# Kernel tuning notes

Hardware: AMD Instinct MI355X
Metric: run time of the kernel (lower is better)

Reference implementation:

```python
import jax, jax.numpy as jnp
import numpy as np

NEG_BIG = -9e15
ALPHA = 0.2  # leakyrelu slope


def setup_inputs() -> dict:
    key = jax.random.key(0)
    k1, k2, k3, k4 = jax.random.split(key, 4)
    N, Fin, Fout = 8192, 256, 256
    input = jax.random.normal(k1, (N, Fin), dtype=jnp.float32)
    adj = jax.random.randint(k2, (N, N), 0, 2, dtype=jnp.int32)
    W = jax.random.normal(k3, (Fin, Fout), dtype=jnp.float32) * (1.0 / np.sqrt(Fin))
    a = jax.random.normal(k4, (2 * Fout, 1), dtype=jnp.float32) * (1.0 / np.sqrt(Fout))
    return {"input": input, "adj": adj, "W": W, "a": a}


def reference(input, adj, W, a):
    # h: [N, F]
    h = input @ W
    Fout = h.shape[1]
    # Fused score: e_ij = leakyrelu(h_i . a[:F] + h_j . a[F:])
    s1 = h @ a[:Fout, 0]   # [N]
    s2 = h @ a[Fout:, 0]   # [N]
    e = s1[:, None] + s2[None, :]            # [N, N]
    e = jnp.where(e >= 0, e, ALPHA * e)      # leaky relu
    e = jnp.where(adj > 0, e, NEG_BIG)       # mask
    attention = jax.nn.softmax(e, axis=1)    # row softmax
    h_prime = attention @ h                  # [N, F]
    return jax.nn.elu(h_prime)               # concat=True -> elu
```

## Files before the change

### kernel.cpp

```cpp
#include <hip/hip_runtime.h>
#include <hip/hip_bf16.h>

#define LRALPHA 0.2f
#define LOG2E 1.4426950408889634f

typedef __attribute__((ext_vector_type(8))) short frag_ab;
typedef __attribute__((ext_vector_type(16))) float f32x16;
typedef float fv4 __attribute__((ext_vector_type(4)));
typedef unsigned int uv4 __attribute__((ext_vector_type(4)));

static __device__ __forceinline__ unsigned short f2bf(float f) {
  __hip_bfloat16 b = __float2bfloat16(f);
  unsigned short u;
  __builtin_memcpy(&u, &b, 2);
  return u;
}

#if __has_builtin(__builtin_amdgcn_exp2f)
#define EXP2F(x) __builtin_amdgcn_exp2f(x)
#else
#define EXP2F(x) exp2f(x)
#endif

static __device__ __forceinline__ unsigned cvt_pk_bf16(float lo, float hi) {
  unsigned r;
  asm("v_cvt_pk_bf16_f32 %0, %1, %2" : "=v"(r) : "v"(lo), "v"(hi));
  return r;
}

static __device__ __forceinline__ frag_ab make_w8(unsigned mb, fv4 sa, fv4 sb,
                                                  float s1r, float mr, float& zloc) {
  float w[8];
#pragma unroll
  for (int e = 0; e < 8; ++e) {
    const float sv = (e < 4) ? sa[e] : sb[e - 4];
    float ee = s1r + sv;
    ee = fmaxf(ee, LRALPHA * ee);
    const float arg = ((mb >> e) & 1u) ? (ee - mr) : -200.f;
    const float ww = EXP2F(arg);
    zloc += ww;
    w[e] = ww;
  }
  uv4 u;
  u[0] = cvt_pk_bf16(w[0], w[1]);
  u[1] = cvt_pk_bf16(w[2], w[3]);
  u[2] = cvt_pk_bf16(w[4], w[5]);
  u[3] = cvt_pk_bf16(w[6], w[7]);
  frag_ab a;
  __builtin_memcpy(&a, &u, 16);
  return a;
}

__global__ __launch_bounds__(256) void gat_adjpack(
    const int* __restrict__ adj, unsigned long long* __restrict__ mask) {
  const int lane = threadIdx.x & 63;
  const int wid = (blockIdx.x * 256 + threadIdx.x) >> 6;
  const int NW = (2048 * 256) >> 6;
  const int NWORDS = (8192 * 8192) / 64;
  for (int w0 = wid * 4; w0 < NWORDS; w0 += NW * 4) {
    int v0 = __builtin_nontemporal_load(&adj[(size_t)(w0 + 0) * 64 + lane]);
    int v1 = __builtin_nontemporal_load(&adj[(size_t)(w0 + 1) * 64 + lane]);
    int v2 = __builtin_nontemporal_load(&adj[(size_t)(w0 + 2) * 64 + lane]);
    int v3 = __builtin_nontemporal_load(&adj[(size_t)(w0 + 3) * 64 + lane]);
    unsigned long long m0 = __ballot(v0 > 0);
    unsigned long long m1 = __ballot(v1 > 0);
    unsigned long long m2 = __ballot(v2 > 0);
    unsigned long long m3 = __ballot(v3 > 0);
    if (lane == 0) {
      mask[w0 + 0] = m0; mask[w0 + 1] = m1;
      mask[w0 + 2] = m2; mask[w0 + 3] = m3;
    }
  }
}

__global__ __launch_bounds__(256, 4) void gat_hproj(
    const float* __restrict__ X, const float* __restrict__ W,
    const float* __restrict__ avec,
    float* __restrict__ s1, float* __restrict__ s2,
    unsigned short* __restrict__ hT) {
  const int tid = threadIdx.x;
  const int row0 = blockIdx.x * 16;
  const float* Xb = X + (size_t)row0 * 256;
  const int c = tid;

  float acc[16];
#pragma unroll
  for (int r = 0; r < 16; ++r) acc[r] = 0.f;

  for (int k = 0; k < 256; k += 4) {
    const float w0 = W[(k + 0) * 256 + c];
    const float w1 = W[(k + 1) * 256 + c];
    const float w2 = W[(k + 2) * 256 + c];
    const float w3 = W[(k + 3) * 256 + c];
#pragma unroll
    for (int r = 0; r < 16; ++r) {
      acc[r] = fmaf(Xb[r * 256 + k + 0], w0, acc[r]);
      acc[r] = fmaf(Xb[r * 256 + k + 1], w1, acc[r]);
      acc[r] = fmaf(Xb[r * 256 + k + 2], w2, acc[r]);
      acc[r] = fmaf(Xb[r * 256 + k + 3], w3, acc[r]);
    }
  }

  alignas(16) unsigned short hu[16];
#pragma unroll
  for (int r = 0; r < 16; ++r) hu[r] = f2bf(acc[r]);
  uv4* hdst = (uv4*)(hT + (size_t)c * 8192 + row0);
  hdst[0] = *(const uv4*)&hu[0];
  hdst[1] = *(const uv4*)&hu[8];

  const float a1c = avec[c];
  const float a2c = avec[256 + c];
  const int lane = tid & 63, wave = tid >> 6;
  __shared__ float r1[4][16], r2[4][16];
#pragma unroll
  for (int r = 0; r < 16; ++r) {
    float v1 = acc[r] * a1c;
    float v2 = acc[r] * a2c;
#pragma unroll
    for (int off = 32; off > 0; off >>= 1) {
      v1 += __shfl_down(v1, off);
      v2 += __shfl_down(v2, off);
    }
    if (lane == 0) { r1[wave][r] = v1; r2[wave][r] = v2; }
  }
  __syncthreads();
  if (tid < 16) {
    s1[row0 + tid] = (r1[0][tid] + r1[1][tid] + r1[2][tid] + r1[3][tid]) * LOG2E;
    s2[row0 + tid] = (r2[0][tid] + r2[1][tid] + r2[2][tid] + r2[3][tid]) * LOG2E;
  }
}

__global__ __launch_bounds__(256, 3) void gat_attn_part(
    const unsigned char* __restrict__ maskB, const unsigned short* __restrict__ hT,
    const float* __restrict__ s1, const float* __restrict__ s2,
    float* __restrict__ pacc, float* __restrict__ pZ) {
  const int bid = blockIdx.x;
  const int rowg = bid >> 2, js = bid & 3;
  const int row0 = rowg * 32;
  const int tid = threadIdx.x;
  const int wave = tid >> 6, lane = tid & 63;
  const int fg = wave & 1, jg = wave >> 1;
  const int ln32 = lane & 31, half = lane >> 5;

  __shared__ float wred[4];
  __shared__ float accL[32][260];
  __shared__ float zL[32];

  float m = -1e30f;
  for (int i = tid; i < 8192; i += 256) m = fmaxf(m, s2[i]);
#pragma unroll
  for (int off = 32; off > 0; off >>= 1) m = fmaxf(m, __shfl_down(m, off));
  if (lane == 0) wred[wave] = m;
  __syncthreads();
  const float s2m = fmaxf(fmaxf(wred[0], wred[1]), fmaxf(wred[2], wred[3]));

  const float s1r = s1[row0 + ln32];
  const float tmv = s1r + s2m;
  const float mr = tmv >= 0.f ? tmv : LRALPHA * tmv;

  const int jbase = (js * 2 + jg) * 1024;
  const unsigned char* mrow = maskB + (size_t)(row0 + ln32) * 1024 + half;
  const unsigned short* hTl = hT + (size_t)(fg * 128 + ln32) * 8192 + half * 8;

  f32x16 acc[4];
#pragma unroll
  for (int ni = 0; ni < 4; ++ni) acc[ni] = (f32x16)(0.f);
  float zloc = 0.f;

  struct LSet { frag_ab B[4]; unsigned mb; fv4 sa, sb; };
  LSet Sa, Sb;

#define LOADSET(S, T)                                                       \
  {                                                                         \
    const int j0_ = jbase + (T) * 16;                                       \
    (S).mb = mrow[j0_ >> 3];                                                \
    const float* sp_ = s2 + j0_ + half * 8;                                 \
    (S).sa = *(const fv4*)sp_;                                              \
    (S).sb = *(const fv4*)(sp_ + 4);                                        \
    _Pragma("unroll")                                                       \
    for (int ni = 0; ni < 4; ++ni)                                          \
      (S).B[ni] = *(const frag_ab*)(hTl + (size_t)ni * 32 * 8192 + j0_);    \
  }

#define USESET(S)                                                           \
  {                                                                         \
    frag_ab A_ = make_w8((S).mb, (S).sa, (S).sb, s1r, mr, zloc);            \
    _Pragma("unroll")                                                       \
    for (int ni = 0; ni < 4; ++ni)                                          \
      acc[ni] = __builtin_amdgcn_mfma_f32_32x32x16_bf16(A_, (S).B[ni],      \
                                                        acc[ni], 0, 0, 0);  \
  }

  LOADSET(Sa, 0);
  for (int t = 0; t < 64; t += 2) {
    LOADSET(Sb, t + 1);
    USESET(Sa);
    LOADSET(Sa, t + 2);
    USESET(Sb);
  }
#undef LOADSET
#undef USESET

  float zrow = zloc + __shfl_xor(zloc, 32);

  if (jg == 0) {
#pragma unroll
    for (int ni = 0; ni < 4; ++ni)
#pragma unroll
      for (int reg = 0; reg < 16; ++reg) {
        const int grow = (reg & 3) + 8 * (reg >> 2) + 4 * half;
        accL[grow][fg * 128 + ni * 32 + ln32] = acc[ni][reg];
      }
    if (fg == 0 && lane < 32) zL[lane] = zrow;
  }
  __syncthreads();
  if (jg == 1) {
    float* paccb = pacc + ((size_t)js * 8192 + row0) * 256;
#pragma unroll
    for (int ni = 0; ni < 4; ++ni)
#pragma unroll
      for (int reg = 0; reg < 16; ++reg) {
        const int grow = (reg & 3) + 8 * (reg >> 2) + 4 * half;
        const int f = fg * 128 + ni * 32 + ln32;
        __builtin_nontemporal_store(acc[ni][reg] + accL[grow][f],
                                    paccb + (size_t)grow * 256 + f);
      }
    if (fg == 0 && lane < 32)
      pZ[js * 8192 + row0 + lane] = zrow + zL[lane];
  }
}

__global__ __launch_bounds__(256) void gat_combine(
    const float* __restrict__ pacc, const float* __restrict__ pZ,
    float* __restrict__ out) {
  const int idx = blockIdx.x * 256 + threadIdx.x;
  const int row = idx >> 6;
  const float z = pZ[row] + pZ[8192 + row] + pZ[16384 + row] + pZ[24576 + row];
  const float invz = 1.f / z;
  const size_t PSTRIDE = (size_t)8192 * 256;
  const fv4 n0 = *(const fv4*)(pacc + (size_t)idx * 4);
  const fv4 n1 = *(const fv4*)(pacc + PSTRIDE + (size_t)idx * 4);
  const fv4 n2 = *(const fv4*)(pacc + 2 * PSTRIDE + (size_t)idx * 4);
  const fv4 n3 = *(const fv4*)(pacc + 3 * PSTRIDE + (size_t)idx * 4);
  fv4 o;
#pragma unroll
  for (int e = 0; e < 4; ++e) {
    const float vsum = (n0[e] + n1[e]) + (n2[e] + n3[e]);
    const float vv = vsum * invz;
    o[e] = vv > 0.f ? vv : expm1f(vv);
  }
  *(fv4*)(out + (size_t)idx * 4) = o;
}

extern "C" void kernel_launch(void* const* d_in, const int* in_sizes, int n_in,
                              void* d_out, int out_size, void* d_ws, size_t ws_size,
                              hipStream_t stream) {
  const float* X = (const float*)d_in[0];
  const int* adj = (const int*)d_in[1];
  const float* W = (const float*)d_in[2];
  const float* avec = (const float*)d_in[3];
  float* out = (float*)d_out;

  float* wsf = (float*)d_ws;
  float* s1 = wsf;
  float* s2 = wsf + 8192;
  float* pZ = wsf + 16384;
  float* pacc = wsf + 49152;
  unsigned short* hT = (unsigned short*)(wsf + 49152 + 8388608);
  unsigned long long* mask =
      (unsigned long long*)(wsf + 49152 + 8388608 + 2097152);

  hipLaunchKernelGGL(gat_adjpack, dim3(2048), dim3(256), 0, stream, adj, mask);
  hipLaunchKernelGGL(gat_hproj, dim3(512), dim3(256), 0, stream, X, W, avec, s1, s2, hT);
  hipLaunchKernelGGL(gat_attn_part, dim3(1024), dim3(256), 0, stream,
                     (const unsigned char*)mask, hT, s1, s2, pacc, pZ);
  hipLaunchKernelGGL(gat_combine, dim3(2048), dim3(256), 0, stream, pacc, pZ, out);
}
```

Before: 592.9 us.

## Transpose adjacency bitmask layout and drop in-block partial reduction

```diff
diff --git a/kernel.cpp b/kernel.cpp
--- a/kernel.cpp
+++ b/kernel.cpp
@@ -51,26 +51,30 @@
   return a;
 }
 
-__global__ __launch_bounds__(256) void gat_adjpack(
-    const int* __restrict__ adj, unsigned long long* __restrict__ mask) {
-  const int lane = threadIdx.x & 63;
-  const int wid = (blockIdx.x * 256 + threadIdx.x) >> 6;
-  const int NW = (2048 * 256) >> 6;
-  const int NWORDS = (8192 * 8192) / 64;
-  for (int w0 = wid * 4; w0 < NWORDS; w0 += NW * 4) {
-    int v0 = __builtin_nontemporal_load(&adj[(size_t)(w0 + 0) * 64 + lane]);
-    int v1 = __builtin_nontemporal_load(&adj[(size_t)(w0 + 1) * 64 + lane]);
-    int v2 = __builtin_nontemporal_load(&adj[(size_t)(w0 + 2) * 64 + lane]);
-    int v3 = __builtin_nontemporal_load(&adj[(size_t)(w0 + 3) * 64 + lane]);
-    unsigned long long m0 = __ballot(v0 > 0);
-    unsigned long long m1 = __ballot(v1 > 0);
-    unsigned long long m2 = __ballot(v2 > 0);
-    unsigned long long m3 = __ballot(v3 > 0);
-    if (lane == 0) {
-      mask[w0 + 0] = m0; mask[w0 + 1] = m1;
-      mask[w0 + 2] = m2; mask[w0 + 3] = m3;
-    }
-  }
+__global__ __launch_bounds__(256) void gat_adjpack_t(
+    const int* __restrict__ adj, unsigned short* __restrict__ maskT) {
+  const int rt = blockIdx.x >> 3;
+  const int jt = blockIdx.x & 7;
+  const int wave = threadIdx.x >> 6, lane = threadIdx.x & 63;
+  __shared__ unsigned short lds[64][64];
+
+  const size_t base = (size_t)rt * 64 * 8192 + jt * 1024 + wave * 256 + lane;
+  for (int r = 0; r < 64; ++r) {
+    const int* ap = adj + base + (size_t)r * 8192;
+#pragma unroll
+    for (int q = 0; q < 4; ++q) {
+      int v = __builtin_nontemporal_load(ap + q * 64);
+      unsigned long long m = __ballot(v > 0);
+      if (lane < 4)
+        lds[wave * 16 + q * 4 + lane][r] = (unsigned short)(m >> (lane * 16));
+    }
+  }
+  __syncthreads();
+  const int jwl = threadIdx.x >> 2, seg = threadIdx.x & 3;
+  unsigned short* dst = maskT + (size_t)(jt * 64 + jwl) * 8192 + rt * 64 + seg * 16;
+  const uv4* src = (const uv4*)&lds[jwl][seg * 16];
+  ((uv4*)dst)[0] = src[0];
+  ((uv4*)dst)[1] = src[1];
 }
 
 __global__ __launch_bounds__(256, 4) void gat_hproj(
@@ -131,7 +135,7 @@
 }
 
 __global__ __launch_bounds__(256, 3) void gat_attn_part(
-    const unsigned char* __restrict__ maskB, const unsigned short* __restrict__ hT,
+    const unsigned short* __restrict__ maskT, const unsigned short* __restrict__ hT,
     const float* __restrict__ s1, const float* __restrict__ s2,
     float* __restrict__ pacc, float* __restrict__ pZ) {
   const int bid = blockIdx.x;
@@ -143,8 +147,6 @@
   const int ln32 = lane & 31, half = lane >> 5;
 
   __shared__ float wred[4];
-  __shared__ float accL[32][260];
-  __shared__ float zL[32];
 
   float m = -1e30f;
   for (int i = tid; i < 8192; i += 256) m = fmaxf(m, s2[i]);
@@ -159,7 +161,8 @@
   const float mr = tmv >= 0.f ? tmv : LRALPHA * tmv;
 
   const int jbase = (js * 2 + jg) * 1024;
-  const unsigned char* mrow = maskB + (size_t)(row0 + ln32) * 1024 + half;
+  const int jwb = jbase >> 4;
+  const unsigned short* mrowT = maskT + row0 + ln32;
   const unsigned short* hTl = hT + (size_t)(fg * 128 + ln32) * 8192 + half * 8;
 
   f32x16 acc[4];
@@ -167,13 +170,15 @@
   for (int ni = 0; ni < 4; ++ni) acc[ni] = (f32x16)(0.f);
   float zloc = 0.f;
 
-  struct LSet { frag_ab B[4]; unsigned mb; fv4 sa, sb; };
+  struct LSet { frag_ab B[4]; unsigned short mw; fv4 sa, sb; };
   LSet Sa, Sb;
 
 #define LOADSET(S, T)                                                       \
   {                                                                         \
     const int j0_ = jbase + (T) * 16;                                       \
-    (S).mb = mrow[j0_ >> 3];                                                \
+    int jw_ = jwb + (T);                                                    \
+    jw_ = jw_ < 512 ? jw_ : 511;              \
+    (S).mw = mrowT[(size_t)jw_ * 8192];                                     \
     const float* sp_ = s2 + j0_ + half * 8;                                 \
     (S).sa = *(const fv4*)sp_;                                              \
     (S).sb = *(const fv4*)(sp_ + 4);                                        \
@@ -184,7 +189,8 @@
 
 #define USESET(S)                                                           \
   {                                                                         \
-    frag_ab A_ = make_w8((S).mb, (S).sa, (S).sb, s1r, mr, zloc);            \
+    const unsigned mb8_ = ((unsigned)(S).mw >> (half * 8)) & 0xffu;         \
+    frag_ab A_ = make_w8(mb8_, (S).sa, (S).sb, s1r, mr, zloc);              \
     _Pragma("unroll")                                                       \
     for (int ni = 0; ni < 4; ++ni)                                          \
       acc[ni] = __builtin_amdgcn_mfma_f32_32x32x16_bf16(A_, (S).B[ni],      \
@@ -201,33 +207,20 @@
 #undef LOADSET
 #undef USESET
 
-  float zrow = zloc + __shfl_xor(zloc, 32);
-
-  if (jg == 0) {
-#pragma unroll
-    for (int ni = 0; ni < 4; ++ni)
-#pragma unroll
-      for (int reg = 0; reg < 16; ++reg) {
-        const int grow = (reg & 3) + 8 * (reg >> 2) + 4 * half;
-        accL[grow][fg * 128 + ni * 32 + ln32] = acc[ni][reg];
-      }
-    if (fg == 0 && lane < 32) zL[lane] = zrow;
-  }
-  __syncthreads();
-  if (jg == 1) {
-    float* paccb = pacc + ((size_t)js * 8192 + row0) * 256;
-#pragma unroll
-    for (int ni = 0; ni < 4; ++ni)
-#pragma unroll
-      for (int reg = 0; reg < 16; ++reg) {
-        const int grow = (reg & 3) + 8 * (reg >> 2) + 4 * half;
-        const int f = fg * 128 + ni * 32 + ln32;
-        __builtin_nontemporal_store(acc[ni][reg] + accL[grow][f],
-                                    paccb + (size_t)grow * 256 + f);
-      }
-    if (fg == 0 && lane < 32)
-      pZ[js * 8192 + row0 + lane] = zrow + zL[lane];
-  }
+  const float zrow = zloc + __shfl_xor(zloc, 32);
+
+  const int slice = js * 2 + jg;
+  float* paccb = pacc + ((size_t)slice * 8192 + row0) * 256;
+#pragma unroll
+  for (int ni = 0; ni < 4; ++ni)
+#pragma unroll
+    for (int reg = 0; reg < 16; ++reg) {
+      const int grow = (reg & 3) + 8 * (reg >> 2) + 4 * half;
+      const int f = fg * 128 + ni * 32 + ln32;
+      __builtin_nontemporal_store(acc[ni][reg], paccb + (size_t)grow * 256 + f);
+    }
+  if (fg == 0 && lane < 32)
+    pZ[slice * 8192 + row0 + lane] = zrow;
 }
 
 __global__ __launch_bounds__(256) void gat_combine(
@@ -235,18 +228,22 @@
     float* __restrict__ out) {
   const int idx = blockIdx.x * 256 + threadIdx.x;
   const int row = idx >> 6;
-  const float z = pZ[row] + pZ[8192 + row] + pZ[16384 + row] + pZ[24576 + row];
+  float z = 0.f;
+#pragma unroll
+  for (int s = 0; s < 8; ++s) z += pZ[s * 8192 + row];
   const float invz = 1.f / z;
   const size_t PSTRIDE = (size_t)8192 * 256;
-  const fv4 n0 = *(const fv4*)(pacc + (size_t)idx * 4);
-  const fv4 n1 = *(const fv4*)(pacc + PSTRIDE + (size_t)idx * 4);
-  const fv4 n2 = *(const fv4*)(pacc + 2 * PSTRIDE + (size_t)idx * 4);
-  const fv4 n3 = *(const fv4*)(pacc + 3 * PSTRIDE + (size_t)idx * 4);
+  fv4 n = {0.f, 0.f, 0.f, 0.f};
+#pragma unroll
+  for (int s = 0; s < 8; ++s) {
+    const fv4 v = *(const fv4*)(pacc + s * PSTRIDE + (size_t)idx * 4);
+#pragma unroll
+    for (int e = 0; e < 4; ++e) n[e] += v[e];
+  }
   fv4 o;
 #pragma unroll
   for (int e = 0; e < 4; ++e) {
-    const float vsum = (n0[e] + n1[e]) + (n2[e] + n3[e]);
-    const float vv = vsum * invz;
+    const float vv = n[e] * invz;
     o[e] = vv > 0.f ? vv : expm1f(vv);
   }
   *(fv4*)(out + (size_t)idx * 4) = o;
@@ -265,14 +262,14 @@
   float* s1 = wsf;
   float* s2 = wsf + 8192;
   float* pZ = wsf + 16384;
-  float* pacc = wsf + 49152;
-  unsigned short* hT = (unsigned short*)(wsf + 49152 + 8388608);
-  unsigned long long* mask =
-      (unsigned long long*)(wsf + 49152 + 8388608 + 2097152);
-
-  hipLaunchKernelGGL(gat_adjpack, dim3(2048), dim3(256), 0, stream, adj, mask);
+  float* pacc = wsf + 81920;
+  unsigned short* hT = (unsigned short*)(wsf + 81920 + 16777216);
+  unsigned short* maskT =
+      (unsigned short*)(wsf + 81920 + 16777216 + 1048576);
+
+  hipLaunchKernelGGL(gat_adjpack_t, dim3(1024), dim3(256), 0, stream, adj, maskT);
   hipLaunchKernelGGL(gat_hproj, dim3(512), dim3(256), 0, stream, X, W, avec, s1, s2, hT);
   hipLaunchKernelGGL(gat_attn_part, dim3(1024), dim3(256), 0, stream,
-                     (const unsigned char*)mask, hT, s1, s2, pacc, pZ);
+                     maskT, hT, s1, s2, pacc, pZ);
   hipLaunchKernelGGL(gat_combine, dim3(2048), dim3(256), 0, stream, pacc, pZ, out);
 }
```

Measured after the change: 672.0 us. 1.13x slower.
